# Kernel optimization log

Hardware: AMD Instinct MI355X
Metric: run time of the kernel (lower is better)

Reference implementation:

```python
import jax, jax.numpy as jnp
import numpy as np
from jax import lax

BATCH = 8192
DIM = 2048
NUM_STATES = 3


def setup_inputs() -> dict:
    key = jax.random.key(0)
    k1, k2, k3, k4 = jax.random.split(key, 4)
    y = jax.random.randint(k1, (BATCH, DIM), 0, 2, dtype=jnp.int64 if jax.config.jax_enable_x64 else jnp.int32)
    transition_probs = jax.random.normal(k2, (NUM_STATES, NUM_STATES), dtype=jnp.float32)
    emission_probs = jax.random.normal(k3, (NUM_STATES, 2), dtype=jnp.float32)
    start_probs = jax.random.normal(k4, (NUM_STATES,), dtype=jnp.float32)
    return {
        "y": y,
        "transition_probs": transition_probs,
        "emission_probs": emission_probs,
        "start_probs": start_probs,
    }


def reference(y, transition_probs, emission_probs, start_probs):
    # Normalize parameters in log space (matches torch.log_softmax)
    log_T = jax.nn.log_softmax(transition_probs, axis=-1)   # [S, S]
    log_E = jax.nn.log_softmax(emission_probs, axis=-1)     # [S, 2]
    log_pi = jax.nn.log_softmax(start_probs, axis=-1)       # [S]

    # Gather per-timestep emission log-probs: [B, DIM, S]
    em = log_E.T[y]

    # alpha_0[b, s] = log_pi[s] + log_E[s, y[b,0]]
    alpha0 = log_pi[None, :] + em[:, 0]                      # [B, S]

    def step(alpha, em_t):
        # alpha[b, i] + log_T[i, j] -> logsumexp over i, plus emission at t
        new = jax.nn.logsumexp(alpha[:, :, None] + log_T[None, :, :], axis=1) + em_t
        return new, None

    # Scan over time: em[:, 1:] moved to leading time axis -> [DIM-1, B, S]
    alpha_T, _ = lax.scan(step, alpha0, jnp.moveaxis(em[:, 1:], 1, 0))

    log_prob = jax.nn.logsumexp(alpha_T, axis=-1)            # [B]
    return log_prob.mean()
```

## Files before the change

### kernel.cpp

```cpp
#include <hip/hip_runtime.h>
#include <math.h>

#define BATCH 8192
#define DIM   2048

__global__ __launch_bounds__(256, 4)
void hmm_fwd(const int* __restrict__ y,
             const float* __restrict__ tp,
             const float* __restrict__ ep,
             const float* __restrict__ sp,
             float* __restrict__ row_lp,
             float* __restrict__ out_atomic)
{
    __shared__ __align__(16) float t4[16 * 12];
    __shared__ __align__(16) float t8[256 * 12];
    __shared__ __align__(16) int   ystage[4][DIM];

    const int tid  = threadIdx.x;
    const int lane = tid & 63;
    const int wid  = tid >> 6;
    const int b    = blockIdx.x * 4 + wid;

    const int* __restrict__ yb = y + (size_t)b * DIM;
    #pragma unroll
    for (int g = 0; g < 8; ++g) {
        int4 v = *reinterpret_cast<const int4*>(yb + g * 256 + lane * 4);
        int Lp = 8*g + (lane >> 3);
        int m  = lane & 7;
        int off = Lp*32 + ((m ^ (Lp & 7)) * 4);
        *reinterpret_cast<int4*>(&ystage[wid][off]) = v;
    }

    float T[3][3], E[3][2], pi[3];
    #pragma unroll
    for (int i = 0; i < 3; ++i) {
        float a0 = tp[i*3+0], a1 = tp[i*3+1], a2 = tp[i*3+2];
        float mx = fmaxf(a0, fmaxf(a1, a2));
        float e0 = __expf(a0-mx), e1 = __expf(a1-mx), e2 = __expf(a2-mx);
        float inv = 1.0f / (e0+e1+e2);
        T[i][0] = e0*inv; T[i][1] = e1*inv; T[i][2] = e2*inv;
    }
    #pragma unroll
    for (int s = 0; s < 3; ++s) {
        float a0 = ep[s*2+0], a1 = ep[s*2+1];
        float mx = fmaxf(a0, a1);
        float e0 = __expf(a0-mx), e1 = __expf(a1-mx);
        float inv = 1.0f / (e0+e1);
        E[s][0] = e0*inv; E[s][1] = e1*inv;
    }
    {
        float a0 = sp[0], a1 = sp[1], a2 = sp[2];
        float mx = fmaxf(a0, fmaxf(a1, a2));
        float e0 = __expf(a0-mx), e1 = __expf(a1-mx), e2 = __expf(a2-mx);
        float inv = 1.0f / (e0+e1+e2);
        pi[0] = e0*inv; pi[1] = e1*inv; pi[2] = e2*inv;
    }

    float v0, v1, v2;
    {
        float c00 =  (T[1][1]*T[2][2] - T[1][2]*T[2][1]);
        float c01 = -(T[1][0]*T[2][2] - T[1][2]*T[2][0]);
        float c02 =  (T[1][0]*T[2][1] - T[1][1]*T[2][0]);
        float c10 = -(T[0][1]*T[2][2] - T[0][2]*T[2][1]);
        float c11 =  (T[0][0]*T[2][2] - T[0][2]*T[2][0]);
        float c12 = -(T[0][0]*T[2][1] - T[0][1]*T[2][0]);
        float c20 =  (T[0][1]*T[1][2] - T[0][2]*T[1][1]);
        float c21 = -(T[0][0]*T[1][2] - T[0][2]*T[1][0]);
        float c22 =  (T[0][0]*T[1][1] - T[0][1]*T[1][0]);
        float det = T[0][0]*c00 + T[0][1]*c01 + T[0][2]*c02;
        float invd = 1.0f / det;
        v0 = (pi[0]*c00 + pi[1]*c01 + pi[2]*c02) * invd;
        v1 = (pi[0]*c10 + pi[1]*c11 + pi[2]*c12) * invd;
        v2 = (pi[0]*c20 + pi[1]*c21 + pi[2]*c22) * invd;
    }

    float M0[9], M1[9];
    #pragma unroll
    for (int k = 0; k < 3; ++k)
        #pragma unroll
        for (int j = 0; j < 3; ++j) {
            M0[k*3+j] = T[k][j] * E[j][0];
            M1[k*3+j] = T[k][j] * E[j][1];
        }

    if (tid < 16) {
        int code = tid;
        float A[9];
        const float* F0 = (code & 1) ? M1 : M0;
        #pragma unroll
        for (int e = 0; e < 9; ++e) A[e] = F0[e];
        code >>= 1;
        for (int s = 1; s < 4; ++s) {
            const float* F = (code & 1) ? M1 : M0;
            code >>= 1;
            float Z[9];
            #pragma unroll
            for (int i = 0; i < 3; ++i)
                #pragma unroll
                for (int j = 0; j < 3; ++j)
                    Z[i*3+j] = fmaf(A[i*3+0], F[0*3+j],
                               fmaf(A[i*3+1], F[1*3+j], A[i*3+2]*F[2*3+j]));
            #pragma unroll
            for (int e = 0; e < 9; ++e) A[e] = Z[e];
        }
        #pragma unroll
        for (int e = 0; e < 9; ++e) t4[tid*12 + e] = A[e];
    }
    __syncthreads();
    {
        const float* A = &t4[(tid & 15) * 12];
        const float* B = &t4[(tid >> 4) * 12];
        float Z[9];
        #pragma unroll
        for (int i = 0; i < 3; ++i)
            #pragma unroll
            for (int j = 0; j < 3; ++j)
                Z[i*3+j] = fmaf(A[i*3+0], B[0*3+j],
                           fmaf(A[i*3+1], B[1*3+j], A[i*3+2]*B[2*3+j]));
        #pragma unroll
        for (int e = 0; e < 9; ++e) t8[tid*12 + e] = Z[e];
    }
    __syncthreads();

    float R[9] = {1.f,0.f,0.f, 0.f,1.f,0.f, 0.f,0.f,1.f};
    float lsc = 0.0f;
    const int lx = lane & 7;
    const int* __restrict__ yrow = &ystage[wid][lane * 32];

    #pragma unroll
    for (int j = 0; j < 4; ++j) {
        int4 a = *reinterpret_cast<const int4*>(yrow + (((2*j)   ^ lx) * 4));
        int4 c = *reinterpret_cast<const int4*>(yrow + (((2*j+1) ^ lx) * 4));
        int idx = a.x + (a.y<<1) + (a.z<<2) + (a.w<<3)
                + (c.x<<4) + (c.y<<5) + (c.z<<6) + (c.w<<7);
        const float4* G4 = reinterpret_cast<const float4*>(&t8[idx * 12]);
        float4 p0 = G4[0], p1 = G4[1], p2 = G4[2];
        float g0 = p0.x, g1 = p0.y, g2 = p0.z,
              g3 = p0.w, g4 = p1.x, g5 = p1.y,
              g6 = p1.z, g7 = p1.w, g8 = p2.x;
        float nR[9];
        #pragma unroll
        for (int i = 0; i < 3; ++i) {
            nR[i*3+0] = fmaf(R[i*3+0], g0, fmaf(R[i*3+1], g3, R[i*3+2]*g6));
            nR[i*3+1] = fmaf(R[i*3+0], g1, fmaf(R[i*3+1], g4, R[i*3+2]*g7));
            nR[i*3+2] = fmaf(R[i*3+0], g2, fmaf(R[i*3+1], g5, R[i*3+2]*g8));
        }
        #pragma unroll
        for (int e = 0; e < 9; ++e) R[e] = nR[e];

        if (j == 1 || j == 3) {
            float m = R[0];
            #pragma unroll
            for (int e = 1; e < 9; ++e) m = fmaxf(m, R[e]);
            lsc += __logf(m);
            float inv = 1.0f / m;
            #pragma unroll
            for (int e = 0; e < 9; ++e) R[e] *= inv;
        }
    }

    #pragma unroll
    for (int o = 1; o < 64; o <<= 1) {
        float S[9];
        #pragma unroll
        for (int e = 0; e < 9; ++e) S[e] = __shfl_down(R[e], o, 64);
        float osc = __shfl_down(lsc, o, 64);
        float nR[9];
        #pragma unroll
        for (int i = 0; i < 3; ++i)
            #pragma unroll
            for (int j = 0; j < 3; ++j)
                nR[i*3+j] = fmaf(R[i*3+0], S[0*3+j],
                            fmaf(R[i*3+1], S[1*3+j], R[i*3+2]*S[2*3+j]));
        #pragma unroll
        for (int e = 0; e < 9; ++e) R[e] = nR[e];
        lsc += osc;
    }

    if (lane == 0) {
        float r0 = R[0] + R[1] + R[2];
        float r1 = R[3] + R[4] + R[5];
        float r2 = R[6] + R[7] + R[8];
        float p  = fmaf(v0, r0, fmaf(v1, r1, v2 * r2));
        float lp = __logf(p) + lsc;
        if (row_lp) row_lp[b] = lp;
        else        atomicAdd(out_atomic, lp * (1.0f / BATCH));
    }
}

__global__ void reduce_mean(const float* __restrict__ row, float* __restrict__ out)
{
    float s = 0.0f;
    for (int i = threadIdx.x; i < BATCH; i += 1024) s += row[i];
    #pragma unroll
    for (int o = 32; o > 0; o >>= 1) s += __shfl_down(s, o, 64);
    __shared__ float sm[16];
    int w = threadIdx.x >> 6;
    if ((threadIdx.x & 63) == 0) sm[w] = s;
    __syncthreads();
    if (threadIdx.x == 0) {
        float t = 0.0f;
        #pragma unroll
        for (int i = 0; i < 16; ++i) t += sm[i];
        out[0] = t * (1.0f / BATCH);
    }
}

extern "C" void kernel_launch(void* const* d_in, const int* in_sizes, int n_in,
                              void* d_out, int out_size, void* d_ws, size_t ws_size,
                              hipStream_t stream)
{
    const int*   y  = (const int*)d_in[0];
    const float* tp = (const float*)d_in[1];
    const float* ep = (const float*)d_in[2];
    const float* sp = (const float*)d_in[3];
    float* out = (float*)d_out;

    const bool use_ws = (ws_size >= BATCH * sizeof(float));
    if (use_ws) {
        float* row = (float*)d_ws;
        hmm_fwd<<<BATCH/4, 256, 0, stream>>>(y, tp, ep, sp, row, nullptr);
        reduce_mean<<<1, 1024, 0, stream>>>(row, out);
    } else {
        hipMemsetAsync(out, 0, sizeof(float), stream);
        hmm_fwd<<<BATCH/4, 256, 0, stream>>>(y, tp, ep, sp, nullptr, out);
    }
}
```

Measured before the change: 104.3 us.

## Pack observations to nibbles in LDS and fuse mean into block atomics

Each lane now keeps its eight int4 loads of y in registers while the parameter setup runs, then packs each int4 into a 4-bit nibble byte in a much smaller LDS stage (512 bytes per wave instead of 8 KB). The scan reads one uint2 per lane and extracts 8-bit table indices with shifts. This cuts LDS footprint and bank traffic and overlaps the global loads with setup math. The separate reduce_mean kernel is replaced by a per-block sum plus one atomicAdd after a memset. That removes a second launch, but atomic float accumulation order is nondeterministic.

```diff
diff --git a/kernel.cpp b/kernel.cpp
--- a/kernel.cpp
+++ b/kernel.cpp
@@ -9,12 +9,12 @@
              const float* __restrict__ tp,
              const float* __restrict__ ep,
              const float* __restrict__ sp,
-             float* __restrict__ row_lp,
-             float* __restrict__ out_atomic)
+             float* __restrict__ out)
 {
     __shared__ __align__(16) float t4[16 * 12];
     __shared__ __align__(16) float t8[256 * 12];
-    __shared__ __align__(16) int   ystage[4][DIM];
+    __shared__ __align__(16) unsigned char ystage[4][512];
+    __shared__ float blk[4];
 
     const int tid  = threadIdx.x;
     const int lane = tid & 63;
@@ -22,13 +22,17 @@
     const int b    = blockIdx.x * 4 + wid;
 
     const int* __restrict__ yb = y + (size_t)b * DIM;
-    #pragma unroll
-    for (int g = 0; g < 8; ++g) {
-        int4 v = *reinterpret_cast<const int4*>(yb + g * 256 + lane * 4);
-        int Lp = 8*g + (lane >> 3);
-        int m  = lane & 7;
-        int off = Lp*32 + ((m ^ (Lp & 7)) * 4);
-        *reinterpret_cast<int4*>(&ystage[wid][off]) = v;
+    int4 v0l, v1l, v2l, v3l, v4l, v5l, v6l, v7l;
+    {
+        const int* p = yb + lane * 4;
+        v0l = *reinterpret_cast<const int4*>(p + 0*256);
+        v1l = *reinterpret_cast<const int4*>(p + 1*256);
+        v2l = *reinterpret_cast<const int4*>(p + 2*256);
+        v3l = *reinterpret_cast<const int4*>(p + 3*256);
+        v4l = *reinterpret_cast<const int4*>(p + 4*256);
+        v5l = *reinterpret_cast<const int4*>(p + 5*256);
+        v6l = *reinterpret_cast<const int4*>(p + 6*256);
+        v7l = *reinterpret_cast<const int4*>(p + 7*256);
     }
 
     float T[3][3], E[3][2], pi[3];
@@ -56,7 +60,7 @@
         pi[0] = e0*inv; pi[1] = e1*inv; pi[2] = e2*inv;
     }
 
-    float v0, v1, v2;
+    float vx, vy, vz;
     {
         float c00 =  (T[1][1]*T[2][2] - T[1][2]*T[2][1]);
         float c01 = -(T[1][0]*T[2][2] - T[1][2]*T[2][0]);
@@ -69,9 +73,9 @@
         float c22 =  (T[0][0]*T[1][1] - T[0][1]*T[1][0]);
         float det = T[0][0]*c00 + T[0][1]*c01 + T[0][2]*c02;
         float invd = 1.0f / det;
-        v0 = (pi[0]*c00 + pi[1]*c01 + pi[2]*c02) * invd;
-        v1 = (pi[0]*c10 + pi[1]*c11 + pi[2]*c12) * invd;
-        v2 = (pi[0]*c20 + pi[1]*c21 + pi[2]*c22) * invd;
+        vx = (pi[0]*c00 + pi[1]*c01 + pi[2]*c02) * invd;
+        vy = (pi[0]*c10 + pi[1]*c11 + pi[2]*c12) * invd;
+        vz = (pi[0]*c20 + pi[1]*c21 + pi[2]*c22) * invd;
     }
 
     float M0[9], M1[9];
@@ -82,6 +86,15 @@
             M0[k*3+j] = T[k][j] * E[j][0];
             M1[k*3+j] = T[k][j] * E[j][1];
         }
+
+    {
+        unsigned char* row = ystage[wid];
+        int4 g[8] = {v0l,v1l,v2l,v3l,v4l,v5l,v6l,v7l};
+        #pragma unroll
+        for (int k = 0; k < 8; ++k)
+            row[64*k + lane] =
+                (unsigned char)(g[k].x | (g[k].y<<1) | (g[k].z<<2) | (g[k].w<<3));
+    }
 
     if (tid < 16) {
         int code = tid;
@@ -90,6 +103,7 @@
         #pragma unroll
         for (int e = 0; e < 9; ++e) A[e] = F0[e];
         code >>= 1;
+        #pragma unroll
         for (int s = 1; s < 4; ++s) {
             const float* F = (code & 1) ? M1 : M0;
             code >>= 1;
@@ -107,9 +121,14 @@
         for (int e = 0; e < 9; ++e) t4[tid*12 + e] = A[e];
     }
     __syncthreads();
-    {
-        const float* A = &t4[(tid & 15) * 12];
-        const float* B = &t4[(tid >> 4) * 12];
+
+    {
+        const float4* A4 = reinterpret_cast<const float4*>(&t4[(tid & 15) * 12]);
+        const float4* B4 = reinterpret_cast<const float4*>(&t4[(tid >> 4) * 12]);
+        float4 a0 = A4[0], a1 = A4[1], a2 = A4[2];
+        float4 b0 = B4[0], b1 = B4[1], b2 = B4[2];
+        float A[9] = {a0.x,a0.y,a0.z, a0.w,a1.x,a1.y, a1.z,a1.w,a2.x};
+        float B[9] = {b0.x,b0.y,b0.z, b0.w,b1.x,b1.y, b1.z,b1.w,b2.x};
         float Z[9];
         #pragma unroll
         for (int i = 0; i < 3; ++i)
@@ -122,17 +141,16 @@
     }
     __syncthreads();
 
+    uint2 q = *reinterpret_cast<const uint2*>(&ystage[wid][8 * lane]);
+
     float R[9] = {1.f,0.f,0.f, 0.f,1.f,0.f, 0.f,0.f,1.f};
     float lsc = 0.0f;
-    const int lx = lane & 7;
-    const int* __restrict__ yrow = &ystage[wid][lane * 32];
 
     #pragma unroll
     for (int j = 0; j < 4; ++j) {
-        int4 a = *reinterpret_cast<const int4*>(yrow + (((2*j)   ^ lx) * 4));
-        int4 c = *reinterpret_cast<const int4*>(yrow + (((2*j+1) ^ lx) * 4));
-        int idx = a.x + (a.y<<1) + (a.z<<2) + (a.w<<3)
-                + (c.x<<4) + (c.y<<5) + (c.z<<6) + (c.w<<7);
+        unsigned w  = (j < 2) ? q.x : q.y;
+        unsigned sh = (j & 1) * 16;
+        int idx = (int)(((w >> sh) & 15u) | ((w >> (sh + 4)) & 0xF0u));
         const float4* G4 = reinterpret_cast<const float4*>(&t8[idx * 12]);
         float4 p0 = G4[0], p1 = G4[1], p2 = G4[2];
         float g0 = p0.x, g1 = p0.y, g2 = p0.z,
@@ -181,28 +199,13 @@
         float r0 = R[0] + R[1] + R[2];
         float r1 = R[3] + R[4] + R[5];
         float r2 = R[6] + R[7] + R[8];
-        float p  = fmaf(v0, r0, fmaf(v1, r1, v2 * r2));
-        float lp = __logf(p) + lsc;
-        if (row_lp) row_lp[b] = lp;
-        else        atomicAdd(out_atomic, lp * (1.0f / BATCH));
-    }
-}
-
-__global__ void reduce_mean(const float* __restrict__ row, float* __restrict__ out)
-{
-    float s = 0.0f;
-    for (int i = threadIdx.x; i < BATCH; i += 1024) s += row[i];
-    #pragma unroll
-    for (int o = 32; o > 0; o >>= 1) s += __shfl_down(s, o, 64);
-    __shared__ float sm[16];
-    int w = threadIdx.x >> 6;
-    if ((threadIdx.x & 63) == 0) sm[w] = s;
+        float p  = fmaf(vx, r0, fmaf(vy, r1, vz * r2));
+        blk[wid] = __logf(p) + lsc;
+    }
     __syncthreads();
-    if (threadIdx.x == 0) {
-        float t = 0.0f;
-        #pragma unroll
-        for (int i = 0; i < 16; ++i) t += sm[i];
-        out[0] = t * (1.0f / BATCH);
+    if (tid == 0) {
+        float s = (blk[0] + blk[1] + blk[2] + blk[3]) * (1.0f / BATCH);
+        atomicAdd(out, s);
     }
 }
 
@@ -216,13 +219,6 @@
     const float* sp = (const float*)d_in[3];
     float* out = (float*)d_out;
 
-    const bool use_ws = (ws_size >= BATCH * sizeof(float));
-    if (use_ws) {
-        float* row = (float*)d_ws;
-        hmm_fwd<<<BATCH/4, 256, 0, stream>>>(y, tp, ep, sp, row, nullptr);
-        reduce_mean<<<1, 1024, 0, stream>>>(row, out);
-    } else {
-        hipMemsetAsync(out, 0, sizeof(float), stream);
-        hmm_fwd<<<BATCH/4, 256, 0, stream>>>(y, tp, ep, sp, nullptr, out);
-    }
+    hipMemsetAsync(out, 0, sizeof(float), stream);
+    hmm_fwd<<<BATCH/4, 256, 0, stream>>>(y, tp, ep, sp, out);
 }
```

Result: slower. 118.7 us (+13.8%).
